# Kernel optimization log

Hardware: AMD Instinct MI355X
Metric: run time of the kernel (lower is better)

Reference implementation:

```python
import jax, jax.numpy as jnp
import numpy as np

N_HEADS = 16
EMB_DIM = 1024
HEAD_DIM = EMB_DIM // N_HEADS


def setup_inputs() -> dict:
    key = jax.random.key(0)
    k1, k2, k3, k4, k5 = jax.random.split(key, 5)
    s = 1.0 / np.sqrt(EMB_DIM)
    return {
        "attn_in": jax.random.normal(k1, (4, 2048, EMB_DIM), dtype=jnp.float32),
        "W_qkv": jax.random.uniform(k2, (EMB_DIM, 3 * EMB_DIM), jnp.float32, -s, s),
        "b_qkv": jax.random.uniform(k3, (3 * EMB_DIM,), jnp.float32, -s, s),
        "W_out": jax.random.uniform(k4, (EMB_DIM, EMB_DIM), jnp.float32, -s, s),
        "b_out": jax.random.uniform(k5, (EMB_DIM,), jnp.float32, -s, s),
    }


def reference(attn_in, W_qkv, b_qkv, W_out, b_out):
    N, L, E = attn_in.shape
    qkv = attn_in @ W_qkv + b_qkv                      # [N, L, 3E]
    q, k, v = jnp.split(qkv, 3, axis=-1)
    # [N, L, E] -> [N, H, L, D]
    def heads(x):
        return x.reshape(N, L, N_HEADS, HEAD_DIM).transpose(0, 2, 1, 3)
    q, k, v = heads(q), heads(k), heads(v)
    scale = 1.0 / np.sqrt(HEAD_DIM)
    scores = jnp.einsum('nhqd,nhkd->nhqk', q, k) * scale   # [N, H, L, L]
    attn = jax.nn.softmax(scores, axis=-1)
    o = jnp.einsum('nhqk,nhkd->nhqd', attn, v)             # [N, H, L, D]
    o = o.transpose(0, 2, 1, 3).reshape(N, L, E)
    return o @ W_out + b_out
```

## Files before the change

### kernel.cpp

```cpp
#include <hip/hip_runtime.h>

typedef __attribute__((ext_vector_type(8))) short short8;
typedef __attribute__((ext_vector_type(4))) float f32x4;
typedef __attribute__((ext_vector_type(16))) float f32x16;

#define MFMA16(A,B,C) __builtin_amdgcn_mfma_f32_16x16x32_bf16(A,B,C,0,0,0)
#define MFMA32(A,B,C) __builtin_amdgcn_mfma_f32_32x32x16_bf16(A,B,C,0,0,0)

__device__ __forceinline__ short f2bf(float f){
  union { float f; unsigned int u; } v; v.f = f;
  unsigned int u = v.u;
  unsigned int r = (u + 0x7fffu + ((u >> 16) & 1u)) >> 16;
  return (short)r;
}

__device__ __forceinline__ unsigned pk2bf(float x, float y){
  unsigned a = __builtin_bit_cast(unsigned, x);
  unsigned b = __builtin_bit_cast(unsigned, y);
  a = a + 0x7fffu + ((a >> 16) & 1u);
  b = b + 0x7fffu + ((b >> 16) & 1u);
  return (a >> 16) | (b & 0xffff0000u);
}

typedef const __attribute__((address_space(1))) void* gptr_t;
typedef __attribute__((address_space(3))) void* lptr_t;

__device__ __forceinline__ void gload16(const short* g, short* l){
  __builtin_amdgcn_global_load_lds((gptr_t)g, (lptr_t)l, 16, 0, 0);
}


__global__ __launch_bounds__(256) void cvt_x_kernel(const float* __restrict__ x,
                                                    short* __restrict__ xb){
  const size_t i = (size_t)blockIdx.x * 256 + threadIdx.x;
  const float4* p = (const float4*)x + i * 2;
  float4 a = p[0], b = p[1];
  short8 o;
  o[0]=f2bf(a.x); o[1]=f2bf(a.y); o[2]=f2bf(a.z); o[3]=f2bf(a.w);
  o[4]=f2bf(b.x); o[5]=f2bf(b.y); o[6]=f2bf(b.z); o[7]=f2bf(b.w);
  *(short8*)(xb + i * 8) = o;
}

__global__ __launch_bounds__(256) void cvt_t_kernel(const float* __restrict__ src,
                                                    short* __restrict__ dst,
                                                    int R, int C){
  __shared__ float tile[32][33];
  const int tx = threadIdx.x, ty = threadIdx.y;
  const int c0 = blockIdx.x * 32, r0 = blockIdx.y * 32;
  #pragma unroll
  for (int i = 0; i < 32; i += 8)
    tile[ty + i][tx] = src[(size_t)(r0 + ty + i) * C + c0 + tx];
  __syncthreads();
  #pragma unroll
  for (int i = 0; i < 32; i += 8)
    dst[(size_t)(c0 + ty + i) * R + r0 + tx] = f2bf(tile[tx][ty + i]);
}


template<int EPI>
__global__ __launch_bounds__(256) void gemm_bt(
    const short* __restrict__ A, const short* __restrict__ BT,
    const float* __restrict__ bias,
    float* __restrict__ Cf,
    short* __restrict__ q_ws, short* __restrict__ k_ws, short* __restrict__ vt_ws)
{
  __shared__ __align__(16) short As[4096];
  __shared__ __align__(16) short Bs[4096];
  const int tid = threadIdx.x;
  const int bm = blockIdx.x, bn = blockIdx.y;
  const int lane = tid & 63, wid = tid >> 6;
  const int wr = wid >> 1, wc = wid & 1;
  const int r = lane & 15, g = lane >> 4;

  f32x4 acc[4][4] = {};

  const short* ag = A  + (size_t)(bm * 128 + (tid >> 2)) * 1024 + (tid & 3) * 8;
  const short* bg = BT + (size_t)(bn * 128 + (tid >> 2)) * 1024 + (tid & 3) * 8;
  short* asd = &As[tid * 8];
  short* bsd = &Bs[tid * 8];

  for (int kk = 0; kk < 32; ++kk){
    gload16(ag + kk * 32,             asd);
    gload16(ag + kk * 32 + 64 * 1024, asd + 2048);
    gload16(bg + kk * 32,             bsd);
    gload16(bg + kk * 32 + 64 * 1024, bsd + 2048);
    asm volatile("s_waitcnt vmcnt(0)" ::: "memory");
    __syncthreads();
    short8 a[4], b[4];
    #pragma unroll
    for (int mf = 0; mf < 4; ++mf)
      a[mf] = *(const short8*)&As[(wr * 64 + mf * 16 + r) * 32 + g * 8];
    #pragma unroll
    for (int nf = 0; nf < 4; ++nf)
      b[nf] = *(const short8*)&Bs[(wc * 64 + nf * 16 + r) * 32 + g * 8];
    #pragma unroll
    for (int mf = 0; mf < 4; ++mf)
      #pragma unroll
      for (int nf = 0; nf < 4; ++nf)
        acc[mf][nf] = MFMA16(a[mf], b[nf], acc[mf][nf]);
    __syncthreads();
  }

  if (EPI == 0){
    #pragma unroll
    for (int nf = 0; nf < 4; ++nf){
      const int c = bn * 128 + wc * 64 + nf * 16 + r;
      const float bv = bias[c];
      const int type = c >> 10;
      const int h = (c & 1023) >> 6, d = c & 63;
      const float mul = (type == 0) ? 0.18033688011112042f : 1.0f;
      #pragma unroll
      for (int mf = 0; mf < 4; ++mf){
        const int row0 = bm * 128 + wr * 64 + mf * 16 + g * 4;
        const int nb = row0 >> 11, l0 = row0 & 2047;
        f32x4 v = acc[mf][nf];
        if (type == 2){
          short4 pk;
          pk.x = f2bf(v[0] + bv); pk.y = f2bf(v[1] + bv);
          pk.z = f2bf(v[2] + bv); pk.w = f2bf(v[3] + bv);
          const int head = nb * 16 + h;
          *(short4*)&vt_ws[(((size_t)head * 32 + (l0 >> 6)) * 64 + d) * 64 + (l0 & 63)] = pk;
        } else {
          short* dst = (type == 0) ? q_ws : k_ws;
          const size_t base = ((size_t)(nb * 16 + h) * 2048 + l0) * 64 + d;
          #pragma unroll
          for (int j = 0; j < 4; ++j)
            dst[base + (size_t)j * 64] = f2bf((v[j] + bv) * mul);
        }
      }
    }
  } else {
    #pragma unroll
    for (int nf = 0; nf < 4; ++nf){
      const int c = bn * 128 + wc * 64 + nf * 16 + r;
      const float bv = bias[c];
      #pragma unroll
      for (int mf = 0; mf < 4; ++mf){
        const int row0 = bm * 128 + wr * 64 + mf * 16 + g * 4;
        f32x4 v = acc[mf][nf];
        #pragma unroll
        for (int j = 0; j < 4; ++j)
          Cf[(size_t)(row0 + j) * 1024 + c] = v[j] + bv;
      }
    }
  }
}


__global__ __launch_bounds__(512, 4) void attn_kernel(
    const short* __restrict__ qw, const short* __restrict__ kw,
    const short* __restrict__ vtw, short* __restrict__ ow)
{
  __shared__ __align__(16) short Ks[4][4096];
  __shared__ __align__(16) short Vs[4][4096];

  const int id = blockIdx.x;
  const int xcd = id & 7, j2 = id >> 3;
  const int nh = xcd * 8 + (j2 & 7);
  const int qt = j2 >> 3;
  const int tid = threadIdx.x;
  const int lane = tid & 63, w = tid >> 6;
  const int l31 = lane & 31, hi = lane >> 5, w7 = lane & 7;

  const size_t hoff = (size_t)nh * 2048 * 64;
  const short* kh = kw + hoff;
  const short* vh = vtw + hoff;

  const int srow = tid >> 3, schunk = tid & 7;
  const int scw = (schunk ^ (srow & 7)) * 8;
  const short* ksrc = kh + srow * 64 + scw;
  const short* vsrc = vh + srow * 64 + scw;

  unsigned aoffh[2][4];
  #pragma unroll
  for (int T = 0; T < 2; ++T)
    #pragma unroll
    for (int s = 0; s < 4; ++s)
      aoffh[T][s] = (unsigned)((l31 + 32 * T) * 64 + (((2 * s + hi) ^ w7) * 8));

  const int qrow0 = qt * 256 + w * 32;
  short8 qfr[4];
  #pragma unroll
  for (int s = 0; s < 4; ++s)
    qfr[s] = *(const short8*)(qw + hoff + (size_t)(qrow0 + l31) * 64 + s * 16 + hi * 8);

  f32x16 oa0 = {}, oa1 = {}, lacc = {};
  short8 onesB;
  #pragma unroll
  for (int i = 0; i < 8; ++i) onesB[i] = (short)0x3F80;

  gload16(ksrc,        &Ks[0][tid * 8]);
  gload16(vsrc,        &Vs[0][tid * 8]);
  gload16(ksrc + 4096, &Ks[1][tid * 8]);
  gload16(vsrc + 4096, &Vs[1][tid * 8]);
  gload16(ksrc + 8192, &Ks[2][tid * 8]);
  gload16(vsrc + 8192, &Vs[2][tid * 8]);

  for (int t4 = 0; t4 < 32; t4 += 4){
    #pragma unroll
    for (int u = 0; u < 4; ++u){
      const int t = t4 + u;
      asm volatile("s_waitcnt vmcnt(4)" ::: "memory");
      asm volatile("s_barrier" ::: "memory");
      {
        const int ts = (t + 3) & 31;
        gload16(ksrc + ts * 4096, &Ks[(u + 3) & 3][tid * 8]);
        gload16(vsrc + ts * 4096, &Vs[(u + 3) & 3][tid * 8]);
      }
      const short* Kb = &Ks[u][0];
      const short* Vb = &Vs[u][0];

      f32x16 ss0, ss1;
      {
        const f32x16 zz = {};
        ss0 = MFMA32(*(const short8*)&Kb[aoffh[0][0]], qfr[0], zz);
        ss1 = MFMA32(*(const short8*)&Kb[aoffh[1][0]], qfr[0], zz);
      }
      #pragma unroll
      for (int s = 1; s < 4; ++s){
        ss0 = MFMA32(*(const short8*)&Kb[aoffh[0][s]], qfr[s], ss0);
        ss1 = MFMA32(*(const short8*)&Kb[aoffh[1][s]], qfr[s], ss1);
      }

      unsigned u0[8], u1[8];
      #pragma unroll
      for (int m = 0; m < 8; ++m){
        u0[m] = pk2bf(__builtin_amdgcn_exp2f(ss0[2 * m]),
                      __builtin_amdgcn_exp2f(ss0[2 * m + 1]));
        u1[m] = pk2bf(__builtin_amdgcn_exp2f(ss1[2 * m]),
                      __builtin_amdgcn_exp2f(ss1[2 * m + 1]));
      }

      short8 pa[4];
      #pragma unroll
      for (int s = 0; s < 4; ++s){
        const int sg = (s & 1) * 4;
        unsigned a0 = (s < 2) ? u0[sg + 0] : u1[sg + 0];
        unsigned a1 = (s < 2) ? u0[sg + 1] : u1[sg + 1];
        unsigned a2 = (s < 2) ? u0[sg + 2] : u1[sg + 2];
        unsigned a3 = (s < 2) ? u0[sg + 3] : u1[sg + 3];
        auto r02 = __builtin_amdgcn_permlane32_swap(a0, a2, false, false);
        auto r13 = __builtin_amdgcn_permlane32_swap(a1, a3, false, false);
        union { unsigned q[4]; short8 s8; } cv;
        cv.q[0] = (unsigned)r02[0]; cv.q[1] = (unsigned)r13[0];
        cv.q[2] = (unsigned)r02[1]; cv.q[3] = (unsigned)r13[1];
        pa[s] = cv.s8;
      }

      #pragma unroll
      for (int s = 0; s < 4; ++s){
        oa0  = MFMA32(pa[s], *(const short8*)&Vb[aoffh[0][s]], oa0);
        oa1  = MFMA32(pa[s], *(const short8*)&Vb[aoffh[1][s]], oa1);
        lacc = MFMA32(pa[s], onesB, lacc);
      }
    }
  }

  const int n = nh >> 4, h = nh & 15;
  #pragma unroll
  for (int j = 0; j < 16; ++j){
    const float inv = 1.0f / lacc[j];
    const int qr = (j & 3) + 8 * (j >> 2) + 4 * hi;
    const size_t base = ((size_t)n * 2048 + qrow0 + qr) * 1024 + h * 64 + l31;
    ow[base]      = f2bf(oa0[j] * inv);
    ow[base + 32] = f2bf(oa1[j] * inv);
  }
}


extern "C" void kernel_launch(void* const* d_in, const int* in_sizes, int n_in,
                              void* d_out, int out_size, void* d_ws, size_t ws_size,
                              hipStream_t stream){
  const float* attn_in = (const float*)d_in[0];
  const float* W_qkv   = (const float*)d_in[1];
  const float* b_qkv   = (const float*)d_in[2];
  const float* W_out   = (const float*)d_in[3];
  const float* b_out   = (const float*)d_in[4];
  float* out = (float*)d_out;

  char* ws = (char*)d_ws;
  short* xb    = (short*)(ws);
  short* wqT   = (short*)(ws + 16777216);
  short* woT   = (short*)(ws + 23068672);
  short* q_ws  = (short*)(ws + 25165824);
  short* k_ws  = (short*)(ws + 41943040);
  short* vt_ws = (short*)(ws + 58720256);
  short* o_ws  = (short*)(ws + 75497472);

  cvt_x_kernel<<<4096, 256, 0, stream>>>(attn_in, xb);
  cvt_t_kernel<<<dim3(96, 32), dim3(32, 8), 0, stream>>>(W_qkv, wqT, 1024, 3072);
  cvt_t_kernel<<<dim3(32, 32), dim3(32, 8), 0, stream>>>(W_out, woT, 1024, 1024);
  gemm_bt<0><<<dim3(64, 24), 256, 0, stream>>>(xb, wqT, b_qkv, nullptr, q_ws, k_ws, vt_ws);
  attn_kernel<<<512, 512, 0, stream>>>(q_ws, k_ws, vt_ws, o_ws);
  gemm_bt<1><<<dim3(64, 8), 256, 0, stream>>>(o_ws, woT, b_out, out, nullptr, nullptr, nullptr);
}
```

Before: 199.2 us.

## Pipeline K/V tiles in pairs to halve barriers in attention loop

The per-tile prefetch with a barrier before each of 32 K/V tiles is replaced by a two-stage pair scheme. Two tiles are loaded while the other two are computed, and the loop waits for all loads and syncs only twice per four tiles. This cuts barrier and wait overhead per tile. In exchange, prefetch distance per tile is shorter and each sync waits for vmcnt(0), which may expose load latency.

After: 197.7 us. About the same (-0.8%).

```diff
diff --git a/kernel.cpp b/kernel.cpp
--- a/kernel.cpp
+++ b/kernel.cpp
@@ -189,71 +189,79 @@
   #pragma unroll
   for (int i = 0; i < 8; ++i) onesB[i] = (short)0x3F80;
 
+  auto compute = [&](const short* Kb, const short* Vb){
+    f32x16 ss0, ss1;
+    {
+      const f32x16 zz = {};
+      ss0 = MFMA32(*(const short8*)&Kb[aoffh[0][0]], qfr[0], zz);
+      ss1 = MFMA32(*(const short8*)&Kb[aoffh[1][0]], qfr[0], zz);
+    }
+    #pragma unroll
+    for (int s = 1; s < 4; ++s){
+      ss0 = MFMA32(*(const short8*)&Kb[aoffh[0][s]], qfr[s], ss0);
+      ss1 = MFMA32(*(const short8*)&Kb[aoffh[1][s]], qfr[s], ss1);
+    }
+
+    unsigned u0[8], u1[8];
+    #pragma unroll
+    for (int m = 0; m < 8; ++m){
+      u0[m] = pk2bf(__builtin_amdgcn_exp2f(ss0[2 * m]),
+                    __builtin_amdgcn_exp2f(ss0[2 * m + 1]));
+      u1[m] = pk2bf(__builtin_amdgcn_exp2f(ss1[2 * m]),
+                    __builtin_amdgcn_exp2f(ss1[2 * m + 1]));
+    }
+
+    short8 pa[4];
+    #pragma unroll
+    for (int s = 0; s < 4; ++s){
+      const int sg = (s & 1) * 4;
+      unsigned a0 = (s < 2) ? u0[sg + 0] : u1[sg + 0];
+      unsigned a1 = (s < 2) ? u0[sg + 1] : u1[sg + 1];
+      unsigned a2 = (s < 2) ? u0[sg + 2] : u1[sg + 2];
+      unsigned a3 = (s < 2) ? u0[sg + 3] : u1[sg + 3];
+      auto r02 = __builtin_amdgcn_permlane32_swap(a0, a2, false, false);
+      auto r13 = __builtin_amdgcn_permlane32_swap(a1, a3, false, false);
+      union { unsigned q[4]; short8 s8; } cv;
+      cv.q[0] = (unsigned)r02[0]; cv.q[1] = (unsigned)r13[0];
+      cv.q[2] = (unsigned)r02[1]; cv.q[3] = (unsigned)r13[1];
+      pa[s] = cv.s8;
+    }
+
+    #pragma unroll
+    for (int s = 0; s < 4; ++s){
+      oa0  = MFMA32(pa[s], *(const short8*)&Vb[aoffh[0][s]], oa0);
+      oa1  = MFMA32(pa[s], *(const short8*)&Vb[aoffh[1][s]], oa1);
+      lacc = MFMA32(pa[s], onesB, lacc);
+    }
+  };
+
   gload16(ksrc,        &Ks[0][tid * 8]);
   gload16(vsrc,        &Vs[0][tid * 8]);
   gload16(ksrc + 4096, &Ks[1][tid * 8]);
   gload16(vsrc + 4096, &Vs[1][tid * 8]);
-  gload16(ksrc + 8192, &Ks[2][tid * 8]);
-  gload16(vsrc + 8192, &Vs[2][tid * 8]);
-
-  for (int t4 = 0; t4 < 32; t4 += 4){
-    #pragma unroll
-    for (int u = 0; u < 4; ++u){
-      const int t = t4 + u;
-      asm volatile("s_waitcnt vmcnt(4)" ::: "memory");
-      asm volatile("s_barrier" ::: "memory");
-      {
-        const int ts = (t + 3) & 31;
-        gload16(ksrc + ts * 4096, &Ks[(u + 3) & 3][tid * 8]);
-        gload16(vsrc + ts * 4096, &Vs[(u + 3) & 3][tid * 8]);
-      }
-      const short* Kb = &Ks[u][0];
-      const short* Vb = &Vs[u][0];
-
-      f32x16 ss0, ss1;
-      {
-        const f32x16 zz = {};
-        ss0 = MFMA32(*(const short8*)&Kb[aoffh[0][0]], qfr[0], zz);
-        ss1 = MFMA32(*(const short8*)&Kb[aoffh[1][0]], qfr[0], zz);
-      }
-      #pragma unroll
-      for (int s = 1; s < 4; ++s){
-        ss0 = MFMA32(*(const short8*)&Kb[aoffh[0][s]], qfr[s], ss0);
-        ss1 = MFMA32(*(const short8*)&Kb[aoffh[1][s]], qfr[s], ss1);
-      }
-
-      unsigned u0[8], u1[8];
-      #pragma unroll
-      for (int m = 0; m < 8; ++m){
-        u0[m] = pk2bf(__builtin_amdgcn_exp2f(ss0[2 * m]),
-                      __builtin_amdgcn_exp2f(ss0[2 * m + 1]));
-        u1[m] = pk2bf(__builtin_amdgcn_exp2f(ss1[2 * m]),
-                      __builtin_amdgcn_exp2f(ss1[2 * m + 1]));
-      }
-
-      short8 pa[4];
-      #pragma unroll
-      for (int s = 0; s < 4; ++s){
-        const int sg = (s & 1) * 4;
-        unsigned a0 = (s < 2) ? u0[sg + 0] : u1[sg + 0];
-        unsigned a1 = (s < 2) ? u0[sg + 1] : u1[sg + 1];
-        unsigned a2 = (s < 2) ? u0[sg + 2] : u1[sg + 2];
-        unsigned a3 = (s < 2) ? u0[sg + 3] : u1[sg + 3];
-        auto r02 = __builtin_amdgcn_permlane32_swap(a0, a2, false, false);
-        auto r13 = __builtin_amdgcn_permlane32_swap(a1, a3, false, false);
-        union { unsigned q[4]; short8 s8; } cv;
-        cv.q[0] = (unsigned)r02[0]; cv.q[1] = (unsigned)r13[0];
-        cv.q[2] = (unsigned)r02[1]; cv.q[3] = (unsigned)r13[1];
-        pa[s] = cv.s8;
-      }
-
-      #pragma unroll
-      for (int s = 0; s < 4; ++s){
-        oa0  = MFMA32(pa[s], *(const short8*)&Vb[aoffh[0][s]], oa0);
-        oa1  = MFMA32(pa[s], *(const short8*)&Vb[aoffh[1][s]], oa1);
-        lacc = MFMA32(pa[s], onesB, lacc);
-      }
-    }
+
+  for (int p = 0; p < 8; ++p){
+    const int t0 = p * 4;
+    asm volatile("s_waitcnt vmcnt(0)" ::: "memory");
+    asm volatile("s_barrier" ::: "memory");
+    gload16(ksrc + (t0 + 2) * 4096, &Ks[2][tid * 8]);
+    gload16(vsrc + (t0 + 2) * 4096, &Vs[2][tid * 8]);
+    gload16(ksrc + (t0 + 3) * 4096, &Ks[3][tid * 8]);
+    gload16(vsrc + (t0 + 3) * 4096, &Vs[3][tid * 8]);
+    compute(&Ks[0][0], &Vs[0][0]);
+    compute(&Ks[1][0], &Vs[1][0]);
+    asm volatile("s_waitcnt vmcnt(0)" ::: "memory");
+    asm volatile("s_barrier" ::: "memory");
+    {
+      const int ts0 = (t0 + 4) & 31;
+      const int ts1 = (t0 + 5) & 31;
+      gload16(ksrc + ts0 * 4096, &Ks[0][tid * 8]);
+      gload16(vsrc + ts0 * 4096, &Vs[0][tid * 8]);
+      gload16(ksrc + ts1 * 4096, &Ks[1][tid * 8]);
+      gload16(vsrc + ts1 * 4096, &Vs[1][tid * 8]);
+    }
+    compute(&Ks[2][0], &Vs[2][0]);
+    compute(&Ks[3][0], &Vs[3][0]);
   }
 
   const int n = nh >> 4, h = nh & 15;
```
